# Performance work log

Hardware: AMD Instinct MI355X
Metric: run time of the kernel (lower is better)

The kernel has to match this reference:

```python
import jax, jax.numpy as jnp
import numpy as np

SW, FB, EMB, H = 96, 64, 512, 3   # seg_width, freq_bandwidth, embedding_dim, num_heads
B, T = 4, 1024
F = SW * FB


def setup_inputs() -> dict:
    key = jax.random.key(0)
    ks = jax.random.split(key, 12)
    s = 0.02
    dh = SW // H
    return {
        "x": jax.random.normal(ks[0], (B, T, F), jnp.float32),
        "o_enc": jax.random.randint(ks[1], (B, T), 0, 2, jnp.int32),
        "r_enc": jax.random.normal(ks[2], (B, T, EMB), jnp.float32),
        "Wq": jax.random.normal(ks[3], (SW, SW), jnp.float32) * s,
        "bq": jnp.zeros((SW,), jnp.float32),
        "Wk": jax.random.normal(ks[4], (SW, SW), jnp.float32) * s,
        "bk": jnp.zeros((SW,), jnp.float32),
        "Wv": jax.random.normal(ks[5], (SW, SW), jnp.float32) * s,
        "bv": jnp.zeros((SW,), jnp.float32),
        "Er": jax.random.normal(ks[6], (FB, dh), jnp.float32) * s,   # relative pos embeddings, max_len = FB
        "W1": jax.random.normal(ks[7], (SW, 4 * SW), jnp.float32) * s,
        "b1": jnp.zeros((4 * SW,), jnp.float32),
        "W2": jax.random.normal(ks[8], (4 * SW, SW), jnp.float32) * s,
        "b2": jnp.zeros((SW,), jnp.float32),
        "We": jax.random.normal(ks[9], (F, EMB), jnp.float32) * s,
        "be": jnp.zeros((EMB,), jnp.float32),
    }


def _skew(qer):
    # qer: (N, h, L, L) -> Srel via Music-Transformer skewing
    padded = jnp.pad(qer, ((0, 0), (0, 0), (0, 0), (1, 0)))      # (N,h,L,L+1)
    n, h, l, l1 = padded.shape
    return padded.reshape(n, h, l1, l)[:, :, 1:, :]               # (N,h,L,L)


def _rel_attention(x, Wq, bq, Wk, bk, Wv, bv, Er):
    # x: (N, L, D); relative global self-attention with causal mask
    N, L, D = x.shape
    dh = D // H

    def heads(t):
        return t.reshape(N, L, H, dh).transpose(0, 2, 1, 3)       # (N,h,L,dh)

    q = heads(x @ Wq + bq)
    k = heads(x @ Wk + bk)
    v = heads(x @ Wv + bv)
    qer = jnp.einsum('nhld,md->nhlm', q, Er)                      # (N,h,L,L)
    srel = _skew(qer)
    scores = (jnp.einsum('nhld,nhmd->nhlm', q, k) + srel) / jnp.sqrt(jnp.asarray(dh, x.dtype))
    causal = jnp.triu(jnp.ones((L, L), bool), 1)
    scores = jnp.where(causal, jnp.finfo(scores.dtype).min, scores)
    attn = jax.nn.softmax(scores, axis=-1)
    out = jnp.einsum('nhlm,nhmd->nhld', attn, v)
    return out.transpose(0, 2, 1, 3).reshape(N, L, D)


def _segmentwise_mean(data, block_ids):
    # data: (B,T,E), block_ids: (B,T) contiguous non-decreasing segment ids in [0,T)
    Bn, Tn, En = data.shape
    seg_sum = jax.vmap(lambda d, i: jax.ops.segment_sum(d, i, num_segments=Tn))(data, block_ids)
    cnt = jax.vmap(lambda i: jax.ops.segment_sum(jnp.ones_like(i), i, num_segments=Tn))(block_ids)
    means = seg_sum / jnp.maximum(cnt, 1).astype(data.dtype)[..., None]
    is_start = jnp.concatenate(
        [jnp.ones((Bn, 1), bool), block_ids[:, 1:] != block_ids[:, :-1]], axis=1)
    gathered = jnp.take_along_axis(means, block_ids[..., None], axis=1)   # (B,T,E)
    # original writes each block's mean only at the block's first position, zeros elsewhere
    return jnp.where(is_start[..., None], gathered, jnp.zeros((), data.dtype))


def reference(x, o_enc, r_enc, Wq, bq, Wk, bk, Wv, bv, Er, W1, b1, W2, b2, We, be):
    Bn, Tn, Fn = x.shape
    xr = x.reshape(Bn * Tn, SW, FB).transpose(0, 2, 1)            # (B*T, FB, SW)
    emb = _rel_attention(xr, Wq, bq, Wk, bk, Wv, bv, Er)
    emb = jax.nn.relu(emb @ W1 + b1) @ W2 + b2                    # FFN: SW -> 4SW -> SW
    emb = emb.transpose(0, 2, 1).reshape(Bn, Tn, Fn)
    emb = emb @ We + be                                           # (B,T,EMB)
    # nn.LayerNorm(emb.shape): normalize over the WHOLE tensor, no affine, eps=1e-8
    mu = emb.mean()
    var = ((emb - mu) ** 2).mean()
    emb = (emb - mu) / jnp.sqrt(var + 1e-8)
    # _regionalize: block ids from cumsum of binary boundary indicators
    block_ids = jnp.cumsum(o_enc, axis=1)
    block_ids = block_ids - block_ids[:, :1]                      # matches 'if b[0]==1: b -= 1'
    block_means = _segmentwise_mean(emb, block_ids)
    return block_means + r_enc + emb
```

## Files before the change

### kernel.cpp

```cpp
#include <hip/hip_runtime.h>
#include <hip/hip_bf16.h>


typedef __attribute__((ext_vector_type(8))) short bf16x8;
typedef __attribute__((ext_vector_type(4))) float f32x4;

struct PtrTab { const void* p[16]; };

enum : int {
  O_WQT = 0,
  O_BQ  = 9984,
  O_WKT = 10080,
  O_BK  = 20064,
  O_WVT = 20160,
  O_BV  = 30144,
  O_ER  = 30240,
  O_W1T = 32288,
  O_B1  = 72224,
  O_W2C = 72608,
  O_B2  = 118688,
  O_WET = 118784
};

__device__ __forceinline__ float b2f(__hip_bfloat16 v) { return __bfloat162float(v); }
__device__ __forceinline__ __hip_bfloat16 f2b(float v) { return __float2bfloat16(v); }

__device__ __forceinline__ void gload16(const void* g, void* l) {
    __builtin_amdgcn_global_load_lds(
        (const __attribute__((address_space(1))) void*)g,
        (__attribute__((address_space(3))) void*)l, 16, 0, 0);
}

__global__ __launch_bounds__(256) void prep_kernel(PtrTab tab,
                                                   __hip_bfloat16* __restrict__ Wc,
                                                   float* __restrict__ sums)
{
    __shared__ __hip_bfloat16 tile[64][65];
    const int bid = blockIdx.x, tid = threadIdx.x;
    const int kt = bid % 96, nt = bid / 96;
    const float* We = (const float*)tab.p[14];
    const int k0 = kt * 64, n0 = nt * 64;
    for (int e = tid; e < 4096; e += 256) {
        int kk = e >> 6, nn = e & 63;
        tile[nn][kk] = f2b(We[(size_t)(k0 + kk) * 512 + n0 + nn]);
    }
    __syncthreads();
    __hip_bfloat16* dstT = Wc + O_WET + ((size_t)nt * 96 + kt) * 4096;
    for (int e = tid; e < 4096; e += 256) dstT[e] = tile[e >> 6][e & 63];

    const int g = bid * 256 + tid;
    const int stride = gridDim.x * 256;
    const float* Wq = (const float*)tab.p[3];
    const float* bq = (const float*)tab.p[4];
    const float* Wk = (const float*)tab.p[5];
    const float* bk = (const float*)tab.p[6];
    const float* Wv = (const float*)tab.p[7];
    const float* bv = (const float*)tab.p[8];
    const float* Er = (const float*)tab.p[9];
    const float* W1 = (const float*)tab.p[10];
    const float* b1 = (const float*)tab.p[11];
    const float* W2 = (const float*)tab.p[12];
    const float* b2 = (const float*)tab.p[13];

    for (int t = 0; t < 3; ++t) {
        const float* W = (t == 0 ? Wq : t == 1 ? Wk : Wv);
        __hip_bfloat16* d = Wc + t * 10080;
        for (int i = g; i < 9984; i += stride) {
            int j = i / 104, c = i - j * 104;
            d[i] = (c < 96) ? f2b(W[c * 96 + j]) : f2b(0.0f);
        }
    }
    for (int i = g; i < 96; i += stride) {
        Wc[O_BQ + i] = f2b(bq[i]);
        Wc[O_BK + i] = f2b(bk[i]);
        Wc[O_BV + i] = f2b(bv[i]);
        Wc[O_B2 + i] = f2b(b2[i]);
    }
    for (int i = g; i < 2048; i += stride) Wc[O_ER + i] = f2b(Er[i]);
    for (int i = g; i < 39936; i += stride) {
        int j = i / 104, c = i - j * 104;
        Wc[O_W1T + i] = (c < 96) ? f2b(W1[c * 384 + j]) : f2b(0.0f);
    }
    for (int i = g; i < 384; i += stride) Wc[O_B1 + i] = f2b(b1[i]);
    for (int i = g; i < 46080; i += stride) {
        int kc = i / 3840, r = i - kc * 3840;
        int nn = r / 40, kk = r - nn * 40;
        Wc[O_W2C + i] = (kk < 32) ? f2b(W2[(kc * 32 + kk) * 96 + nn]) : f2b(0.0f);
    }
    if (g < 2) sums[g] = 0.f;
}

__global__ __launch_bounds__(256, 4) void attn_ffn_kernel(
    const float* __restrict__ x, const __hip_bfloat16* __restrict__ Wc,
    __hip_bfloat16* __restrict__ M)
{
    const int n = blockIdx.x, tid = threadIdx.x;
    const int w = tid >> 6, lane = tid & 63, quad = lane >> 4, ln = lane & 15;

    __shared__ __align__(16) char smem[40448];
    __hip_bfloat16* xs  = (__hip_bfloat16*)(smem);
    __hip_bfloat16* wb  = (__hip_bfloat16*)(smem);
    __hip_bfloat16* kS  = (__hip_bfloat16*)(smem + 13312);
    __hip_bfloat16* vT  = (__hip_bfloat16*)(smem + 26624);
    __hip_bfloat16* hid = (__hip_bfloat16*)(smem + 13312);

    const f32x4 z4 = {0.f, 0.f, 0.f, 0.f};
    const int rowb = 16 * w + quad * 4;

    bf16x8 wf[9], wfn[9];
    #pragma unroll
    for (int i = 0; i < 9; ++i)
        wf[i] = *(const bf16x8*)(Wc + O_WQT + ((i % 3) * 16 + ln) * 104 + (i / 3) * 32 + quad * 8);

    {
        const float* xb = x + (size_t)n * 6144;
        const int sb = w * 24;
        for (int c = 0; c < 3; ++c) {
            float v[8];
            #pragma unroll
            for (int j = 0; j < 8; ++j) v[j] = xb[(sb + c * 8 + j) * 64 + lane];
            union { __hip_bfloat16 h[8]; bf16x8 v8; } pk;
            #pragma unroll
            for (int j = 0; j < 8; ++j) pk.h[j] = f2b(v[j]);
            *(bf16x8*)(xs + lane * 104 + sb + c * 8) = pk.v8;
        }
    }
    __syncthreads();

    bf16x8 af[3];
    #pragma unroll
    for (int ks = 0; ks < 3; ++ks)
        af[ks] = *(const bf16x8*)(xs + (16 * w + ln) * 104 + ks * 32 + quad * 8);

    bf16x8 aqr[3];

    for (int st = 0; st < 6; ++st) {
        const int t = st >> 1, half = st & 1;
        if (st < 5) {
            const __hip_bfloat16* nb = Wc + ((st + 1) >> 1) * 10080 + ((st + 1) & 1) * 4992;
            #pragma unroll
            for (int i = 0; i < 9; ++i)
                wfn[i] = *(const bf16x8*)(nb + ((i % 3) * 16 + ln) * 104 + (i / 3) * 32 + quad * 8);
        }
        f32x4 acc[3] = {z4, z4, z4};
        #pragma unroll
        for (int ks = 0; ks < 3; ++ks)
            #pragma unroll
            for (int ct = 0; ct < 3; ++ct)
                acc[ct] = __builtin_amdgcn_mfma_f32_16x16x32_bf16(af[ks], wf[ks * 3 + ct], acc[ct], 0, 0, 0);
        const int j0 = half * 48;
        const __hip_bfloat16* bt = Wc + 9984 + t * 10080;
        #pragma unroll
        for (int ct = 0; ct < 3; ++ct) {
            int col = j0 + ct * 16 + ln;
            float bb = b2f(bt[col]);
            if (t < 2) {
                #pragma unroll
                for (int r = 0; r < 4; ++r)
                    kS[(rowb + r) * 104 + col] = f2b(acc[ct][r] + bb);
            } else {
                union { __hip_bfloat16 h4[4]; uint2 u; } pk;
                #pragma unroll
                for (int r = 0; r < 4; ++r) pk.h4[r] = f2b(acc[ct][r] + bb);
                *(uint2*)(vT + col * 72 + rowb) = pk.u;
            }
        }
        if (t == 0 && half == 1) {
            #pragma unroll
            for (int h = 0; h < 3; ++h)
                aqr[h] = *(const bf16x8*)(kS + (16 * w + ln) * 104 + h * 32 + quad * 8);
        }
        #pragma unroll
        for (int i = 0; i < 9; ++i) wf[i] = wfn[i];
    }

    bf16x8 erf[4];
    #pragma unroll
    for (int tn = 0; tn < 4; ++tn)
        erf[tn] = *(const bf16x8*)(Wc + O_ER + (16 * tn + ln) * 32 + quad * 8);
    __syncthreads();

    bf16x8 pf0, pf1, pf2;
    {
        const bf16x8* src = (const bf16x8*)(Wc + O_W1T);
        pf0 = src[tid]; pf1 = src[tid + 256];
        if (tid + 512 < 624) pf2 = src[tid + 512];
    }

    __hip_bfloat16* S2 = xs + 32;
    const int ql = 16 * w + ln;
    const int sshift = 63 - ql;
    f32x4 oacc[3][2] = {{z4, z4}, {z4, z4}, {z4, z4}};

    #pragma unroll
    for (int h = 0; h < 3; ++h) {
        const int c0 = h * 32;
        bf16x8 aq = aqr[h];
        #pragma unroll
        for (int tn = 0; tn < 4; ++tn) {
            f32x4 q4 = __builtin_amdgcn_mfma_f32_16x16x32_bf16(erf[tn], aq, z4, 0, 0, 0);
            #pragma unroll
            for (int r = 0; r < 4; ++r) {
                int e = 16 * tn + 4 * quad + r;
                if (e >= sshift) S2[ql * 104 + (e - sshift)] = f2b(q4[r]);
            }
        }
        float sco[4][4];
        #pragma unroll
        for (int tn = 0; tn < 4; ++tn) {
            bf16x8 kf = *(const bf16x8*)(kS + (16 * tn + ln) * 104 + c0 + quad * 8);
            f32x4 s1 = __builtin_amdgcn_mfma_f32_16x16x32_bf16(kf, aq, z4, 0, 0, 0);
            #pragma unroll
            for (int r = 0; r < 4; ++r) sco[tn][r] = s1[r];
        }
        #pragma unroll
        for (int tn = 0; tn < 4; ++tn) {
            union { __hip_bfloat16 h4[4]; uint2 u; } sr;
            sr.u = *(const uint2*)(S2 + ql * 104 + 16 * tn + 4 * quad);
            #pragma unroll
            for (int r = 0; r < 4; ++r) {
                int m = 16 * tn + 4 * quad + r;
                sco[tn][r] = (m <= ql)
                    ? (sco[tn][r] + b2f(sr.h4[r])) * 0.17677669529663687f
                    : -3.0e38f;
            }
        }
        float mt[4];
        #pragma unroll
        for (int tn = 0; tn < 4; ++tn)
            mt[tn] = fmaxf(fmaxf(sco[tn][0], sco[tn][1]), fmaxf(sco[tn][2], sco[tn][3]));
        float mx = fmaxf(fmaxf(mt[0], mt[1]), fmaxf(mt[2], mt[3]));
        mx = fmaxf(mx, __shfl_xor(mx, 16, 64));
        mx = fmaxf(mx, __shfl_xor(mx, 32, 64));
        float st_[4];
        #pragma unroll
        for (int tn = 0; tn < 4; ++tn) {
            #pragma unroll
            for (int r = 0; r < 4; ++r) sco[tn][r] = __expf(sco[tn][r] - mx);
            st_[tn] = (sco[tn][0] + sco[tn][1]) + (sco[tn][2] + sco[tn][3]);
        }
        float sum = (st_[0] + st_[1]) + (st_[2] + st_[3]);
        sum += __shfl_xor(sum, 16, 64);
        sum += __shfl_xor(sum, 32, 64);
        const float inv = 1.0f / sum;
        #pragma unroll
        for (int tn = 0; tn < 4; ++tn) {
            union { __hip_bfloat16 h4[4]; uint2 u; } pk;
            #pragma unroll
            for (int r = 0; r < 4; ++r) pk.h4[r] = f2b(sco[tn][r] * inv);
            *(uint2*)(S2 + ql * 104 + 16 * tn + 4 * quad) = pk.u;
        }
        #pragma unroll
        for (int ks2 = 0; ks2 < 2; ++ks2) {
            bf16x8 pa = *(const bf16x8*)(S2 + ql * 104 + ks2 * 32 + quad * 8);
            #pragma unroll
            for (int t2 = 0; t2 < 2; ++t2) {
                bf16x8 vb = *(const bf16x8*)(vT + (c0 + 16 * t2 + ln) * 72 + ks2 * 32 + quad * 8);
                oacc[h][t2] = __builtin_amdgcn_mfma_f32_16x16x32_bf16(pa, vb, oacc[h][t2], 0, 0, 0);
            }
        }
    }
    #pragma unroll
    for (int h = 0; h < 3; ++h)
        #pragma unroll
        for (int t2 = 0; t2 < 2; ++t2)
            #pragma unroll
            for (int r = 0; r < 4; ++r)
                xs[(rowb + r) * 104 + h * 32 + 16 * t2 + ln] = f2b(oacc[h][t2][r]);

    bf16x8 cf[3];
    #pragma unroll
    for (int ks = 0; ks < 3; ++ks)
        cf[ks] = *(const bf16x8*)(xs + (16 * w + ln) * 104 + ks * 32 + quad * 8);

    f32x4 acc2[6] = {z4, z4, z4, z4, z4, z4};
    bf16x8 w2f[6], w2fn[6];
    for (int jh = 0; jh < 2; ++jh) {
        for (int cc = 0; cc < 4; ++cc) {
            const int j0g = jh * 192 + cc * 48;
            __syncthreads();
            {
                bf16x8* dst = (bf16x8*)wb;
                dst[tid] = pf0;
                dst[tid + 256] = pf1;
                if (tid + 512 < 624) dst[tid + 512] = pf2;
                if (cc < 3) {
                    const bf16x8* src = (const bf16x8*)(Wc + O_W1T + jh * 19968 + (cc + 1) * 4992);
                    pf0 = src[tid]; pf1 = src[tid + 256];
                    if (tid + 512 < 624) pf2 = src[tid + 512];
                } else {
                    const __hip_bfloat16* nb = Wc + O_W2C + (jh * 6) * 3840;
                    #pragma unroll
                    for (int ct = 0; ct < 6; ++ct)
                        w2f[ct] = *(const bf16x8*)(nb + (ct * 16 + ln) * 40 + quad * 8);
                }
            }
            __syncthreads();
            f32x4 a1[3] = {z4, z4, z4};
            #pragma unroll
            for (int ks = 0; ks < 3; ++ks) {
                #pragma unroll
                for (int ct = 0; ct < 3; ++ct) {
                    bf16x8 b = *(const bf16x8*)(wb + (ct * 16 + ln) * 104 + ks * 32 + quad * 8);
                    a1[ct] = __builtin_amdgcn_mfma_f32_16x16x32_bf16(cf[ks], b, a1[ct], 0, 0, 0);
                }
            }
            #pragma unroll
            for (int ct = 0; ct < 3; ++ct) {
                int colg = j0g + ct * 16 + ln;
                int coll = cc * 48 + ct * 16 + ln;
                float bb = b2f(Wc[O_B1 + colg]);
                #pragma unroll
                for (int r = 0; r < 4; ++r)
                    hid[(rowb + r) * 200 + coll] = f2b(fmaxf(a1[ct][r] + bb, 0.f));
            }
        }
        for (int kc = 0; kc < 6; ++kc) {
            if (kc < 5) {
                const __hip_bfloat16* nb = Wc + O_W2C + (jh * 6 + kc + 1) * 3840;
                #pragma unroll
                for (int ct = 0; ct < 6; ++ct)
                    w2fn[ct] = *(const bf16x8*)(nb + (ct * 16 + ln) * 40 + quad * 8);
            } else if (jh == 0) {
                const bf16x8* src = (const bf16x8*)(Wc + O_W1T + 19968);
                pf0 = src[tid]; pf1 = src[tid + 256];
                if (tid + 512 < 624) pf2 = src[tid + 512];
            }
            bf16x8 a = *(const bf16x8*)(hid + (16 * w + ln) * 200 + kc * 32 + quad * 8);
            #pragma unroll
            for (int ct = 0; ct < 6; ++ct)
                acc2[ct] = __builtin_amdgcn_mfma_f32_16x16x32_bf16(a, w2f[ct], acc2[ct], 0, 0, 0);
            if (kc < 5) {
                #pragma unroll
                for (int ct = 0; ct < 6; ++ct) w2f[ct] = w2fn[ct];
            }
        }
    }

    __hip_bfloat16* Mg = M + (size_t)n * 6144;
    #pragma unroll
    for (int ct = 0; ct < 6; ++ct) {
        int d = ct * 16 + ln;
        float bb = b2f(Wc[O_B2 + d]);
        union { __hip_bfloat16 h4[4]; uint2 u; } pk;
        #pragma unroll
        for (int r = 0; r < 4; ++r) pk.h4[r] = f2b(acc2[ct][r] + bb);
        *(uint2*)((char*)Mg + (size_t)(d * 64 + rowb) * 2) = pk.u;
    }
}

__global__ __launch_bounds__(256) void gemm_kernel(
    const __hip_bfloat16* __restrict__ A,
    const __hip_bfloat16* __restrict__ Wc,
    const float* __restrict__ be,
    float* __restrict__ Y,
    float* __restrict__ sums)
{
    __shared__ __align__(16) char gsm[65536];
    const int row0 = blockIdx.x * 64, nt = blockIdx.y, col0 = nt * 64;
    const int tid = threadIdx.x;
    const int w = tid >> 6, lane = tid & 63, quad = lane >> 4, ln = lane & 15;
    const __hip_bfloat16* Bsrc = Wc + O_WET + (size_t)nt * 96 * 4096;

    const f32x4 z4 = {0.f, 0.f, 0.f, 0.f};
    f32x4 acc[4] = {z4, z4, z4, z4};

    auto stage = [&](int buf, int kt) {
        char* Ab = gsm + buf * 16384;
        char* Bb = gsm + 32768 + buf * 16384;
        #pragma unroll
        for (int j = 0; j < 4; ++j) {
            const int b = j * 4096 + tid * 16;
            const int row = b >> 8;
            const int s = b ^ ((row & 7) << 4);
            const int col = (s & 255) >> 1;
            gload16(A + (size_t)(row0 + row) * 6144 + kt * 128 + col,
                    Ab + j * 4096 + w * 1024);
            gload16(Bsrc + (size_t)(2 * kt + (col >> 6)) * 4096 + row * 64 + (col & 63),
                    Bb + j * 4096 + w * 1024);
        }
    };

    stage(0, 0);
    __syncthreads();

    for (int kt = 0; kt < 48; ++kt) {
        const int cur = kt & 1;
        if (kt < 47) stage(cur ^ 1, kt + 1);
        const char* Ab = gsm + cur * 16384;
        const char* Bb = gsm + 32768 + cur * 16384;
        #pragma unroll
        for (int ks = 0; ks < 4; ++ks) {
            const int ra = ((16 * w + ln) << 8) + ks * 64 + quad * 16;
            bf16x8 a = *(const bf16x8*)(Ab + (ra ^ ((ln & 7) << 4)));
            #pragma unroll
            for (int tn = 0; tn < 4; ++tn) {
                const int rb = ((16 * tn + ln) << 8) + ks * 64 + quad * 16;
                bf16x8 b = *(const bf16x8*)(Bb + (rb ^ ((ln & 7) << 4)));
                acc[tn] = __builtin_amdgcn_mfma_f32_16x16x32_bf16(a, b, acc[tn], 0, 0, 0);
            }
        }
        __syncthreads();
    }

    float s = 0.f, s2 = 0.f;
    #pragma unroll
    for (int tn = 0; tn < 4; ++tn) {
        int col = col0 + 16 * tn + ln;
        float bb = be[col];
        #pragma unroll
        for (int r = 0; r < 4; ++r) {
            float v = acc[tn][r] + bb;
            Y[(size_t)(row0 + 16 * w + quad * 4 + r) * 512 + col] = v;
            s += v; s2 += v * v;
        }
    }
    #pragma unroll
    for (int off = 1; off < 64; off <<= 1) {
        s  += __shfl_xor(s, off, 64);
        s2 += __shfl_xor(s2, off, 64);
    }
    float* r1s = (float*)gsm;
    float* r2s = r1s + 4;
    if (lane == 0) { r1s[w] = s; r2s[w] = s2; }
    __syncthreads();
    if (tid == 0) {
        atomicAdd(&sums[0], r1s[0] + r1s[1] + r1s[2] + r1s[3]);
        atomicAdd(&sums[1], r2s[0] + r2s[1] + r2s[2] + r2s[3]);
    }
}

__global__ __launch_bounds__(256) void segid_kernel(const int* __restrict__ o_enc,
                                                    int* __restrict__ bids) {
    __shared__ int ts[256];
    const int b = blockIdx.x, tid = threadIdx.x;
    const int* o = o_enc + b * 1024;
    int v0 = o[4 * tid], v1 = o[4 * tid + 1], v2 = o[4 * tid + 2], v3 = o[4 * tid + 3];
    int p0 = v0, p1 = p0 + v1, p2 = p1 + v2, p3 = p2 + v3;
    ts[tid] = p3;
    __syncthreads();
    for (int off = 1; off < 256; off <<= 1) {
        int mine = ts[tid];
        int add = (tid >= off) ? ts[tid - off] : 0;
        __syncthreads();
        ts[tid] = mine + add;
        __syncthreads();
    }
    const int excl = (tid > 0) ? ts[tid - 1] : 0;
    const int off0 = o[0];
    int* bid = bids + b * 1024;
    bid[4 * tid]     = excl + p0 - off0;
    bid[4 * tid + 1] = excl + p1 - off0;
    bid[4 * tid + 2] = excl + p2 - off0;
    bid[4 * tid + 3] = excl + p3 - off0;
}

__global__ __launch_bounds__(256) void final_kernel(
    const float* __restrict__ Y, const int* __restrict__ bids,
    const float* __restrict__ sums, const float* __restrict__ r_enc,
    float* __restrict__ out)
{
    const int bt = blockIdx.x;
    const int b = bt >> 10, t = bt & 1023;
    const float mu = sums[0] * (1.0f / 2097152.0f);
    const float var = sums[1] * (1.0f / 2097152.0f) - mu * mu;
    const float rstd = rsqrtf(var + 1e-8f);
    const int* bid = bids + b * 1024;
    const int my = bid[t];
    const bool is_start = (t == 0) || (bid[t - 1] != my);
    int t2 = t + 1;
    float invc = 0.f;
    if (is_start) {
        while (t2 < 1024 && bid[t2] == my) ++t2;
        invc = 1.0f / (float)(t2 - t);
    }
    for (int e = threadIdx.x; e < 512; e += 256) {
        const size_t base = (size_t)bt * 512 + e;
        float res = (Y[base] - mu) * rstd + r_enc[base];
        if (is_start) {
            float s = 0.f;
            for (int tt = t; tt < t2; ++tt)
                s += (Y[((size_t)(b * 1024 + tt)) * 512 + e] - mu) * rstd;
            res += s * invc;
        }
        out[base] = res;
    }
}

extern "C" void kernel_launch(void* const* d_in, const int* in_sizes, int n_in,
                              void* d_out, int out_size, void* d_ws, size_t ws_size,
                              hipStream_t stream) {
    PtrTab tab;
    for (int i = 0; i < 16; ++i) tab.p[i] = d_in[i];

    char* ws = (char*)d_ws;
    __hip_bfloat16* M  = (__hip_bfloat16*)ws;
    float* Y           = (float*)(ws + 50331648);
    float* sums        = (float*)(ws + 58720256);
    int*   bids        = (int*)(ws + 58720320);
    __hip_bfloat16* Wc = (__hip_bfloat16*)(ws + 58736768);

    prep_kernel<<<768, 256, 0, stream>>>(tab, Wc, sums);
    attn_ffn_kernel<<<4096, 256, 0, stream>>>((const float*)d_in[0], Wc, M);
    gemm_kernel<<<dim3(64, 8), 256, 0, stream>>>(M, Wc, (const float*)d_in[15], Y, sums);
    segid_kernel<<<4, 256, 0, stream>>>((const int*)d_in[1], bids);
    final_kernel<<<4096, 256, 0, stream>>>(Y, bids, sums, (const float*)d_in[2], (float*)d_out);
}
```

Baseline: 374.2 us.

## Swap MFMA operand order for packed LDS stores and fold segment-id scan into prep

In the attention/FFN kernel, several MFMAs now take their operands in swapped order, so each lane holds four consecutive columns of one row. The Q/K projection, attention output and FFN hidden stores can then be written to LDS as packed 8-byte stores instead of four scalar 2-byte stores, and bias loads are vectorised to match. The block-id cumsum kernel is folded into the first four blocks of the prep kernel, removing one kernel launch. This adds serial scan work to those four prep blocks and relies on the transposed accumulator layout being consistent with every consumer.

New measurement: 371.5 us. Within noise of the previous version (-0.7%).

```diff
diff --git a/kernel.cpp b/kernel.cpp
--- a/kernel.cpp
+++ b/kernel.cpp
@@ -33,7 +33,8 @@
 
 __global__ __launch_bounds__(256) void prep_kernel(PtrTab tab,
                                                    __hip_bfloat16* __restrict__ Wc,
-                                                   float* __restrict__ sums)
+                                                   float* __restrict__ sums,
+                                                   int* __restrict__ bids)
 {
     __shared__ __hip_bfloat16 tile[64][65];
     const int bid = blockIdx.x, tid = threadIdx.x;
@@ -88,6 +89,30 @@
         Wc[O_W2C + i] = (kk < 32) ? f2b(W2[(kc * 32 + kk) * 96 + nn]) : f2b(0.0f);
     }
     if (g < 2) sums[g] = 0.f;
+
+    if (bid < 4) {
+        __syncthreads();
+        int* ts = (int*)tile;
+        const int* o = (const int*)tab.p[1] + bid * 1024;
+        int v0 = o[4 * tid], v1 = o[4 * tid + 1], v2 = o[4 * tid + 2], v3 = o[4 * tid + 3];
+        int p0 = v0, p1 = p0 + v1, p2 = p1 + v2, p3 = p2 + v3;
+        ts[tid] = p3;
+        __syncthreads();
+        for (int off = 1; off < 256; off <<= 1) {
+            int mine = ts[tid];
+            int add = (tid >= off) ? ts[tid - off] : 0;
+            __syncthreads();
+            ts[tid] = mine + add;
+            __syncthreads();
+        }
+        const int excl = (tid > 0) ? ts[tid - 1] : 0;
+        const int off0 = o[0];
+        int* bd = bids + bid * 1024;
+        bd[4 * tid]     = excl + p0 - off0;
+        bd[4 * tid + 1] = excl + p1 - off0;
+        bd[4 * tid + 2] = excl + p2 - off0;
+        bd[4 * tid + 3] = excl + p3 - off0;
+    }
 }
 
 __global__ __launch_bounds__(256, 4) void attn_ffn_kernel(
@@ -106,6 +131,7 @@
 
     const f32x4 z4 = {0.f, 0.f, 0.f, 0.f};
     const int rowb = 16 * w + quad * 4;
+    const int myrow = 16 * w + ln;
 
     bf16x8 wf[9], wfn[9];
     #pragma unroll
@@ -130,7 +156,7 @@
     bf16x8 af[3];
     #pragma unroll
     for (int ks = 0; ks < 3; ++ks)
-        af[ks] = *(const bf16x8*)(xs + (16 * w + ln) * 104 + ks * 32 + quad * 8);
+        af[ks] = *(const bf16x8*)(xs + myrow * 104 + ks * 32 + quad * 8);
 
     bf16x8 aqr[3];
 
@@ -143,22 +169,34 @@
                 wfn[i] = *(const bf16x8*)(nb + ((i % 3) * 16 + ln) * 104 + (i / 3) * 32 + quad * 8);
         }
         f32x4 acc[3] = {z4, z4, z4};
-        #pragma unroll
-        for (int ks = 0; ks < 3; ++ks)
-            #pragma unroll
-            for (int ct = 0; ct < 3; ++ct)
-                acc[ct] = __builtin_amdgcn_mfma_f32_16x16x32_bf16(af[ks], wf[ks * 3 + ct], acc[ct], 0, 0, 0);
         const int j0 = half * 48;
         const __hip_bfloat16* bt = Wc + 9984 + t * 10080;
-        #pragma unroll
-        for (int ct = 0; ct < 3; ++ct) {
-            int col = j0 + ct * 16 + ln;
-            float bb = b2f(bt[col]);
-            if (t < 2) {
-                #pragma unroll
-                for (int r = 0; r < 4; ++r)
-                    kS[(rowb + r) * 104 + col] = f2b(acc[ct][r] + bb);
-            } else {
+        if (t < 2) {
+            #pragma unroll
+            for (int ks = 0; ks < 3; ++ks)
+                #pragma unroll
+                for (int ct = 0; ct < 3; ++ct)
+                    acc[ct] = __builtin_amdgcn_mfma_f32_16x16x32_bf16(wf[ks * 3 + ct], af[ks], acc[ct], 0, 0, 0);
+            #pragma unroll
+            for (int ct = 0; ct < 3; ++ct) {
+                const int cb = j0 + ct * 16 + 4 * quad;
+                union { uint2 u; __hip_bfloat16 h[4]; } bu;
+                bu.u = *(const uint2*)(bt + cb);
+                union { __hip_bfloat16 h4[4]; uint2 u; } pk;
+                #pragma unroll
+                for (int r = 0; r < 4; ++r) pk.h4[r] = f2b(acc[ct][r] + b2f(bu.h[r]));
+                *(uint2*)(kS + myrow * 104 + cb) = pk.u;
+            }
+        } else {
+            #pragma unroll
+            for (int ks = 0; ks < 3; ++ks)
+                #pragma unroll
+                for (int ct = 0; ct < 3; ++ct)
+                    acc[ct] = __builtin_amdgcn_mfma_f32_16x16x32_bf16(af[ks], wf[ks * 3 + ct], acc[ct], 0, 0, 0);
+            #pragma unroll
+            for (int ct = 0; ct < 3; ++ct) {
+                int col = j0 + ct * 16 + ln;
+                float bb = b2f(bt[col]);
                 union { __hip_bfloat16 h4[4]; uint2 u; } pk;
                 #pragma unroll
                 for (int r = 0; r < 4; ++r) pk.h4[r] = f2b(acc[ct][r] + bb);
@@ -168,7 +206,7 @@
         if (t == 0 && half == 1) {
             #pragma unroll
             for (int h = 0; h < 3; ++h)
-                aqr[h] = *(const bf16x8*)(kS + (16 * w + ln) * 104 + h * 32 + quad * 8);
+                aqr[h] = *(const bf16x8*)(kS + myrow * 104 + h * 32 + quad * 8);
         }
         #pragma unroll
         for (int i = 0; i < 9; ++i) wf[i] = wfn[i];
@@ -188,7 +226,7 @@
     }
 
     __hip_bfloat16* S2 = xs + 32;
-    const int ql = 16 * w + ln;
+    const int ql = myrow;
     const int sshift = 63 - ql;
     f32x4 oacc[3][2] = {{z4, z4}, {z4, z4}, {z4, z4}};
 
@@ -256,22 +294,24 @@
             #pragma unroll
             for (int t2 = 0; t2 < 2; ++t2) {
                 bf16x8 vb = *(const bf16x8*)(vT + (c0 + 16 * t2 + ln) * 72 + ks2 * 32 + quad * 8);
-                oacc[h][t2] = __builtin_amdgcn_mfma_f32_16x16x32_bf16(pa, vb, oacc[h][t2], 0, 0, 0);
+                oacc[h][t2] = __builtin_amdgcn_mfma_f32_16x16x32_bf16(vb, pa, oacc[h][t2], 0, 0, 0);
             }
         }
     }
     #pragma unroll
     for (int h = 0; h < 3; ++h)
         #pragma unroll
-        for (int t2 = 0; t2 < 2; ++t2)
-            #pragma unroll
-            for (int r = 0; r < 4; ++r)
-                xs[(rowb + r) * 104 + h * 32 + 16 * t2 + ln] = f2b(oacc[h][t2][r]);
+        for (int t2 = 0; t2 < 2; ++t2) {
+            union { __hip_bfloat16 h4[4]; uint2 u; } pk;
+            #pragma unroll
+            for (int r = 0; r < 4; ++r) pk.h4[r] = f2b(oacc[h][t2][r]);
+            *(uint2*)(xs + myrow * 104 + h * 32 + 16 * t2 + 4 * quad) = pk.u;
+        }
 
     bf16x8 cf[3];
     #pragma unroll
     for (int ks = 0; ks < 3; ++ks)
-        cf[ks] = *(const bf16x8*)(xs + (16 * w + ln) * 104 + ks * 32 + quad * 8);
+        cf[ks] = *(const bf16x8*)(xs + myrow * 104 + ks * 32 + quad * 8);
 
     f32x4 acc2[6] = {z4, z4, z4, z4, z4, z4};
     bf16x8 w2f[6], w2fn[6];
@@ -302,17 +342,19 @@
                 #pragma unroll
                 for (int ct = 0; ct < 3; ++ct) {
                     bf16x8 b = *(const bf16x8*)(wb + (ct * 16 + ln) * 104 + ks * 32 + quad * 8);
-                    a1[ct] = __builtin_amdgcn_mfma_f32_16x16x32_bf16(cf[ks], b, a1[ct], 0, 0, 0);
+                    a1[ct] = __builtin_amdgcn_mfma_f32_16x16x32_bf16(b, cf[ks], a1[ct], 0, 0, 0);
                 }
             }
             #pragma unroll
             for (int ct = 0; ct < 3; ++ct) {
-                int colg = j0g + ct * 16 + ln;
-                int coll = cc * 48 + ct * 16 + ln;
-                float bb = b2f(Wc[O_B1 + colg]);
+                const int cb = ct * 16 + 4 * quad;
+                union { uint2 u; __hip_bfloat16 h[4]; } bu;
+                bu.u = *(const uint2*)(Wc + O_B1 + j0g + cb);
+                union { __hip_bfloat16 h4[4]; uint2 u; } pk;
                 #pragma unroll
                 for (int r = 0; r < 4; ++r)
-                    hid[(rowb + r) * 200 + coll] = f2b(fmaxf(a1[ct][r] + bb, 0.f));
+                    pk.h4[r] = f2b(fmaxf(a1[ct][r] + b2f(bu.h[r]), 0.f));
+                *(uint2*)(hid + myrow * 200 + cc * 48 + cb) = pk.u;
             }
         }
         for (int kc = 0; kc < 6; ++kc) {
@@ -326,7 +368,7 @@
                 pf0 = src[tid]; pf1 = src[tid + 256];
                 if (tid + 512 < 624) pf2 = src[tid + 512];
             }
-            bf16x8 a = *(const bf16x8*)(hid + (16 * w + ln) * 200 + kc * 32 + quad * 8);
+            bf16x8 a = *(const bf16x8*)(hid + myrow * 200 + kc * 32 + quad * 8);
             #pragma unroll
             for (int ct = 0; ct < 6; ++ct)
                 acc2[ct] = __builtin_amdgcn_mfma_f32_16x16x32_bf16(a, w2f[ct], acc2[ct], 0, 0, 0);
@@ -428,31 +470,6 @@
         atomicAdd(&sums[0], r1s[0] + r1s[1] + r1s[2] + r1s[3]);
         atomicAdd(&sums[1], r2s[0] + r2s[1] + r2s[2] + r2s[3]);
     }
-}
-
-__global__ __launch_bounds__(256) void segid_kernel(const int* __restrict__ o_enc,
-                                                    int* __restrict__ bids) {
-    __shared__ int ts[256];
-    const int b = blockIdx.x, tid = threadIdx.x;
-    const int* o = o_enc + b * 1024;
-    int v0 = o[4 * tid], v1 = o[4 * tid + 1], v2 = o[4 * tid + 2], v3 = o[4 * tid + 3];
-    int p0 = v0, p1 = p0 + v1, p2 = p1 + v2, p3 = p2 + v3;
-    ts[tid] = p3;
-    __syncthreads();
-    for (int off = 1; off < 256; off <<= 1) {
-        int mine = ts[tid];
-        int add = (tid >= off) ? ts[tid - off] : 0;
-        __syncthreads();
-        ts[tid] = mine + add;
-        __syncthreads();
-    }
-    const int excl = (tid > 0) ? ts[tid - 1] : 0;
-    const int off0 = o[0];
-    int* bid = bids + b * 1024;
-    bid[4 * tid]     = excl + p0 - off0;
-    bid[4 * tid + 1] = excl + p1 - off0;
-    bid[4 * tid + 2] = excl + p2 - off0;
-    bid[4 * tid + 3] = excl + p3 - off0;
 }
 
 __global__ __launch_bounds__(256) void final_kernel(
@@ -500,9 +517,8 @@
     int*   bids        = (int*)(ws + 58720320);
     __hip_bfloat16* Wc = (__hip_bfloat16*)(ws + 58736768);
 
-    prep_kernel<<<768, 256, 0, stream>>>(tab, Wc, sums);
+    prep_kernel<<<768, 256, 0, stream>>>(tab, Wc, sums, bids);
     attn_ffn_kernel<<<4096, 256, 0, stream>>>((const float*)d_in[0], Wc, M);
     gemm_kernel<<<dim3(64, 8), 256, 0, stream>>>(M, Wc, (const float*)d_in[15], Y, sums);
-    segid_kernel<<<4, 256, 0, stream>>>((const int*)d_in[1], bids);
     final_kernel<<<4096, 256, 0, stream>>>(Y, bids, sums, (const float*)d_in[2], (float*)d_out);
 }
```
